# Kernel tuning notes

Measured on AMD Instinct MI355X. Metric: run time of the kernel, lower is better.

The kernel has to match this reference:

```python
import jax, jax.numpy as jnp
import numpy as np

EPS = 1e-5

def _bn(z, g, b):
    # train-mode BatchNorm2d: batch stats over (B,H,W), biased variance
    mean = z.mean(axis=(0, 2, 3), keepdims=True)
    var = z.var(axis=(0, 2, 3), keepdims=True)
    return g[None, :, None, None] * (z - mean) * jax.lax.rsqrt(var + EPS) + b[None, :, None, None]

def _conv1x1(x, w):
    # x: [B,C,H,W], w: [O,C] -> [B,O,H,W]
    return jnp.einsum('bchw,oc->bohw', x, w)

def _proj(x, w1, g1, b1, w2, g2, b2):
    z = _bn(_conv1x1(x, w1), g1, b1)
    return _bn(_conv1x1(z, w2), g2, b2)

def setup_inputs() -> dict:
    key = jax.random.key(0)
    ks = jax.random.split(key, 24)
    B, Cx, Cy, M, H, W = 4, 512, 256, 64, 64, 64
    f32 = jnp.float32
    def wmat(k, o, c):
        return jax.random.normal(k, (o, c), f32) * (c ** -0.5)
    def gamma(k, c):
        return 1.0 + 0.1 * jax.random.normal(k, (c,), f32)
    def beta(k, c):
        return 0.1 * jax.random.normal(k, (c,), f32)
    inp = {
        'x': jax.random.normal(ks[0], (B, Cx, H, W), f32),
        'y': jax.random.normal(ks[1], (B, Cy, H, W), f32),
        # f_self
        'ws1': wmat(ks[2], M, Cx), 'gs1': gamma(ks[3], M), 'bs1': beta(ks[4], M),
        'ws2': wmat(ks[5], M, M),  'gs2': gamma(ks[6], M), 'bs2': beta(ks[7], M),
        # f_x
        'wx1': wmat(ks[8], M, Cx), 'gx1': gamma(ks[9], M), 'bx1': beta(ks[10], M),
        'wx2': wmat(ks[11], M, M), 'gx2': gamma(ks[12], M), 'bx2': beta(ks[13], M),
        # f_y
        'wy1': wmat(ks[14], M, Cy), 'gy1': gamma(ks[15], M), 'by1': beta(ks[16], M),
        'wy2': wmat(ks[17], M, M),  'gy2': gamma(ks[18], M), 'by2': beta(ks[19], M),
        # f_up
        'wu': wmat(ks[20], Cx, M), 'gu': gamma(ks[21], Cx), 'bu': beta(ks[22], Cx),
    }
    return inp

def reference(x, y, ws1, gs1, bs1, ws2, gs2, bs2,
              wx1, gx1, bx1, wx2, gx2, bx2,
              wy1, gy1, by1, wy2, gy2, by2,
              wu, gu, bu):
    B, C, H, W = x.shape
    M = ws1.shape[0]
    N = H * W
    fself = _proj(x, ws1, gs1, bs1, ws2, gs2, bs2).reshape(B, M, N).transpose(0, 2, 1)  # [B,N,M]
    fx = _proj(x, wx1, gx1, bx1, wx2, gx2, bx2).reshape(B, M, N).transpose(0, 2, 1)      # [B,N,M]
    fy = _proj(y, wy1, gy1, by1, wy2, gy2, by2).reshape(B, M, N)                          # [B,M,N]
    sim = jnp.matmul(fx, fy)                  # [B,N,N]  (scale=False)
    attn = jax.nn.softmax(sim, axis=-1)
    fout = jnp.matmul(attn, fself)            # [B,N,M]
    fout = fout.transpose(0, 2, 1).reshape(B, M, H, W)
    out = _bn(_conv1x1(fout, wu), gu, bu)
    return x + out
```

## Files before the change

kernel.cpp:

```cpp
#include <hip/hip_runtime.h>
#include <hip/hip_fp16.h>
#include <cstdint>

constexpr int N_ = 4096;
constexpr float CNT = 16384.f;

typedef __attribute__((ext_vector_type(8))) _Float16 half8;
typedef __attribute__((ext_vector_type(4))) float f32x4;
union fragh { half8 h8; int i4[4]; };

__device__ inline int pkh(float a, float b) {
  union { __half2 h; int i; } u;
  u.h = __float22half2_rn(float2{a, b});
  return u.i;
}


__global__ __launch_bounds__(256) void conv1_k(
    const float* __restrict__ x, const float* __restrict__ y,
    const float* __restrict__ ws1, const float* __restrict__ wx1,
    const float* __restrict__ wy1,
    float* __restrict__ z1s, float* __restrict__ z1x, float* __restrict__ z1y,
    float* __restrict__ stats) {
  const int t = threadIdx.x;
  const int slice = blockIdx.x;
  const int b = slice >> 5;
  const int n0 = (slice & 31) * 128;
  const int branch = blockIdx.y;
  const float* A = branch == 2 ? y : x;
  const float* W = branch == 0 ? ws1 : (branch == 1 ? wx1 : wy1);
  float* out = branch == 0 ? z1s : (branch == 1 ? z1x : z1y);
  const int K = branch == 2 ? 256 : 512;
  float* st = stats + branch * 128;

  __shared__ float sA[32][132];
  __shared__ float sW[32][72];

  const int to = (t >> 5) * 8;
  const int tn = (t & 31) * 4;
  float acc[8][4];
#pragma unroll
  for (int i = 0; i < 8; ++i)
#pragma unroll
    for (int j = 0; j < 4; ++j) acc[i][j] = 0.f;

  const float* Ab = A + (size_t)b * K * N_ + n0;
#pragma unroll 1
  for (int k0 = 0; k0 < K; k0 += 32) {
    __syncthreads();
#pragma unroll
    for (int i = 0; i < 4; ++i) {
      int row = i * 8 + (t >> 5);
      float4 v = *(const float4*)&Ab[(size_t)(k0 + row) * N_ + tn];
      *(float4*)&sA[row][tn] = v;
    }
    {
      int o = t >> 2, kk = (t & 3) * 8;
      float4 w0 = *(const float4*)&W[(size_t)o * K + k0 + kk];
      float4 w1 = *(const float4*)&W[(size_t)o * K + k0 + kk + 4];
      sW[kk + 0][o] = w0.x; sW[kk + 1][o] = w0.y;
      sW[kk + 2][o] = w0.z; sW[kk + 3][o] = w0.w;
      sW[kk + 4][o] = w1.x; sW[kk + 5][o] = w1.y;
      sW[kk + 6][o] = w1.z; sW[kk + 7][o] = w1.w;
    }
    __syncthreads();
#pragma unroll
    for (int k = 0; k < 32; ++k) {
      float4 a = *(const float4*)&sA[k][tn];
      float4 w0 = *(const float4*)&sW[k][to];
      float4 w1 = *(const float4*)&sW[k][to + 4];
      float wv[8] = {w0.x, w0.y, w0.z, w0.w, w1.x, w1.y, w1.z, w1.w};
      float av[4] = {a.x, a.y, a.z, a.w};
#pragma unroll
      for (int i = 0; i < 8; ++i)
#pragma unroll
        for (int j = 0; j < 4; ++j) acc[i][j] += wv[i] * av[j];
    }
  }
  float* Cb = out + (size_t)b * 64 * N_ + n0;
#pragma unroll
  for (int i = 0; i < 8; ++i) {
    float4 v = {acc[i][0], acc[i][1], acc[i][2], acc[i][3]};
    *(float4*)&Cb[(size_t)(to + i) * N_ + tn] = v;
  }
#pragma unroll
  for (int i = 0; i < 8; ++i) {
    float s = acc[i][0] + acc[i][1] + acc[i][2] + acc[i][3];
    float q = acc[i][0] * acc[i][0] + acc[i][1] * acc[i][1] +
              acc[i][2] * acc[i][2] + acc[i][3] * acc[i][3];
#pragma unroll
    for (int d = 1; d < 32; d <<= 1) { s += __shfl_xor(s, d); q += __shfl_xor(q, d); }
    if ((t & 31) == 0) { atomicAdd(&st[to + i], s); atomicAdd(&st[64 + to + i], q); }
  }
}

__global__ __launch_bounds__(256) void conv2_k(
    const float* __restrict__ z1s, const float* __restrict__ z1x,
    const float* __restrict__ z1y,
    const float* __restrict__ ws2, const float* __restrict__ wx2,
    const float* __restrict__ wy2,
    const float* __restrict__ gs1, const float* __restrict__ bs1,
    const float* __restrict__ gx1, const float* __restrict__ bx1,
    const float* __restrict__ gy1, const float* __restrict__ by1,
    float* __restrict__ z2s, float* __restrict__ z2x, float* __restrict__ z2y,
    float* __restrict__ stats) {
  const int t = threadIdx.x;
  const int slice = blockIdx.x;
  const int b = slice >> 5;
  const int n0 = (slice & 31) * 128;
  const int branch = blockIdx.y;
  const float* A = branch == 0 ? z1s : (branch == 1 ? z1x : z1y);
  const float* W = branch == 0 ? ws2 : (branch == 1 ? wx2 : wy2);
  const float* g1 = branch == 0 ? gs1 : (branch == 1 ? gx1 : gy1);
  const float* b1 = branch == 0 ? bs1 : (branch == 1 ? bx1 : by1);
  float* out = branch == 0 ? z2s : (branch == 1 ? z2x : z2y);
  const float* stin = stats + branch * 128;
  float* stout = stats + (3 + branch) * 128;

  __shared__ float sA[32][132];
  __shared__ float sW[32][72];
  __shared__ float sc[64], sh[64];

  if (t < 64) {
    float mean = stin[t] * (1.f / CNT);
    float var = stin[64 + t] * (1.f / CNT) - mean * mean;
    float r = rsqrtf(var + 1e-5f);
    float s = g1[t] * r;
    sc[t] = s;
    sh[t] = b1[t] - mean * s;
  }

  const int to = (t >> 5) * 8;
  const int tn = (t & 31) * 4;
  float acc[8][4];
#pragma unroll
  for (int i = 0; i < 8; ++i)
#pragma unroll
    for (int j = 0; j < 4; ++j) acc[i][j] = 0.f;

  const float* Ab = A + (size_t)b * 64 * N_ + n0;
#pragma unroll 1
  for (int k0 = 0; k0 < 64; k0 += 32) {
    __syncthreads();
#pragma unroll
    for (int i = 0; i < 4; ++i) {
      int row = i * 8 + (t >> 5);
      float4 v = *(const float4*)&Ab[(size_t)(k0 + row) * N_ + tn];
      float s = sc[k0 + row], h = sh[k0 + row];
      v.x = v.x * s + h; v.y = v.y * s + h; v.z = v.z * s + h; v.w = v.w * s + h;
      *(float4*)&sA[row][tn] = v;
    }
    {
      int o = t >> 2, kk = (t & 3) * 8;
      float4 w0 = *(const float4*)&W[(size_t)o * 64 + k0 + kk];
      float4 w1 = *(const float4*)&W[(size_t)o * 64 + k0 + kk + 4];
      sW[kk + 0][o] = w0.x; sW[kk + 1][o] = w0.y;
      sW[kk + 2][o] = w0.z; sW[kk + 3][o] = w0.w;
      sW[kk + 4][o] = w1.x; sW[kk + 5][o] = w1.y;
      sW[kk + 6][o] = w1.z; sW[kk + 7][o] = w1.w;
    }
    __syncthreads();
#pragma unroll
    for (int k = 0; k < 32; ++k) {
      float4 a = *(const float4*)&sA[k][tn];
      float4 w0 = *(const float4*)&sW[k][to];
      float4 w1 = *(const float4*)&sW[k][to + 4];
      float wv[8] = {w0.x, w0.y, w0.z, w0.w, w1.x, w1.y, w1.z, w1.w};
      float av[4] = {a.x, a.y, a.z, a.w};
#pragma unroll
      for (int i = 0; i < 8; ++i)
#pragma unroll
        for (int j = 0; j < 4; ++j) acc[i][j] += wv[i] * av[j];
    }
  }
  float* Cb = out + (size_t)b * 64 * N_ + n0;
#pragma unroll
  for (int i = 0; i < 8; ++i) {
    float4 v = {acc[i][0], acc[i][1], acc[i][2], acc[i][3]};
    *(float4*)&Cb[(size_t)(to + i) * N_ + tn] = v;
  }
#pragma unroll
  for (int i = 0; i < 8; ++i) {
    float s = acc[i][0] + acc[i][1] + acc[i][2] + acc[i][3];
    float q = acc[i][0] * acc[i][0] + acc[i][1] * acc[i][1] +
              acc[i][2] * acc[i][2] + acc[i][3] * acc[i][3];
#pragma unroll
    for (int d = 1; d < 32; d <<= 1) { s += __shfl_xor(s, d); q += __shfl_xor(q, d); }
    if ((t & 31) == 0) { atomicAdd(&stout[to + i], s); atomicAdd(&stout[64 + to + i], q); }
  }
}

__global__ __launch_bounds__(256) void pack_k(
    const float* __restrict__ z2s, const float* __restrict__ z2x,
    const float* __restrict__ z2y,
    const float* __restrict__ gs2, const float* __restrict__ bs2,
    const float* __restrict__ gx2, const float* __restrict__ bx2,
    const float* __restrict__ gy2, const float* __restrict__ by2,
    int* __restrict__ Qh, int* __restrict__ Kf, int* __restrict__ Vf,
    const float* __restrict__ stats) {
  const int job = blockIdx.z;
  const int idx = blockIdx.x * 256 + threadIdx.x;
  const float* z2 = job == 0 ? z2x : (job == 1 ? z2y : z2s);
  const float* g2 = job == 0 ? gx2 : (job == 1 ? gy2 : gs2);
  const float* b2 = job == 0 ? bx2 : (job == 1 ? by2 : bs2);
  const float* st = stats + (job == 0 ? 4 : (job == 1 ? 5 : 3)) * 128;
  int* outp = job == 0 ? Qh : (job == 1 ? Kf : Vf);

  auto snorm = [&](int c, float& s, float& h) {
    float mean = st[c] * (1.f / CNT);
    float var = st[64 + c] * (1.f / CNT) - mean * mean;
    float r = rsqrtf(var + 1e-5f);
    s = g2[c] * r;
    h = b2[c] - mean * s;
  };
  if (job == 0) {
    int n = idx & 4095, c = (idx >> 12) & 31, b = idx >> 17;
    float s0, h0, s1, h1;
    snorm(2 * c, s0, h0);
    snorm(2 * c + 1, s1, h1);
    float v0 = z2[((size_t)b * 64 + 2 * c) * N_ + n] * s0 + h0;
    float v1 = z2[((size_t)b * 64 + 2 * c + 1) * N_ + n] * s1 + h1;
    outp[idx] = pkh(v0, v1);
  } else if (job == 1) {
    int n = idx & 4095, c = (idx >> 12) & 31, b = idx >> 17;
    float s0, h0, s1, h1;
    snorm(2 * c, s0, h0);
    snorm(2 * c + 1, s1, h1);
    float v0 = z2[((size_t)b * 64 + 2 * c) * N_ + n] * s0 + h0;
    float v1 = z2[((size_t)b * 64 + 2 * c + 1) * N_ + n] * s1 + h1;
    int t16 = n >> 4, la = n & 15, g = c >> 4, quad = (c & 15) >> 2, jj = c & 3;
    outp[(((b * 256 + t16) * 2 + g) * 64 + quad * 16 + la) * 4 + jj] = pkh(v0, v1);
  } else {
    int k = idx & 2047, ch = (idx >> 11) & 63, b = idx >> 17;
    float s0, h0;
    snorm(ch, s0, h0);
    float2 v = *(const float2*)&z2[((size_t)b * 64 + ch) * N_ + 2 * k];
    int kb = k >> 4, p = k & 15, quad = p >> 2, w = p & 3, mt = ch >> 4, la = ch & 15;
    outp[(((b * 128 + kb) * 4 + mt) * 64 + quad * 16 + la) * 4 + w] =
        pkh(v.x * s0 + h0, v.y * s0 + h0);
  }
}

__global__ __launch_bounds__(256, 4) void attn_k(const int* __restrict__ Qh,
                                                 const int* __restrict__ Kf,
                                                 const int* __restrict__ Vf,
                                                 float* __restrict__ fout) {
  const int tid = threadIdx.x;
  const int lane = tid & 63;
  const int wid = tid >> 6;
  const int la = lane & 15;
  const int quad = lane >> 4;
  const int b = blockIdx.x & 3;
  const int qbase = (blockIdx.x >> 2) * 16;
  const int* Qb = Qh + (size_t)b * 32 * N_;
  const int* Kb4 = Kf + (size_t)b * 131072;
  const int* Vb4 = Vf + (size_t)b * 131072;

  __shared__ union USm {
    int P16[4][16 * 20];
    struct { float O[4][16][69]; float M[4][16]; float L[4][16]; } e;
  } smu;
  int* myP = smu.P16[wid];

  fragh aq[2];
#pragma unroll
  for (int c = 0; c < 2; ++c)
#pragma unroll
    for (int j = 0; j < 4; ++j)
      aq[c].i4[j] = Qb[(size_t)(c * 16 + quad * 4 + j) * N_ + qbase + la];

  f32x4 o[4];
  float mrun = -3.0e38f, lrun = 0.f;
#pragma unroll
  for (int mt = 0; mt < 4; ++mt) o[mt] = f32x4{0.f, 0.f, 0.f, 0.f};

  const int jbeg = wid * (N_ / 4);
  const int jend = jbeg + N_ / 4;

  int4 ka[2][2], kb2[2][2];
#pragma unroll
  for (int nt = 0; nt < 2; ++nt)
#pragma unroll
    for (int g = 0; g < 2; ++g)
      ka[nt][g] = *(const int4*)&Kb4[((((jbeg >> 4) + nt) * 2 + g) * 64 + lane) * 4];

  auto body = [&](int j0, int4 (&kc)[2][2], int4 (&kn)[2][2]) {
    f32x4 s[2];
#pragma unroll
    for (int nt = 0; nt < 2; ++nt) {
      fragh k0, k1;
      k0.i4[0] = kc[nt][0].x; k0.i4[1] = kc[nt][0].y;
      k0.i4[2] = kc[nt][0].z; k0.i4[3] = kc[nt][0].w;
      k1.i4[0] = kc[nt][1].x; k1.i4[1] = kc[nt][1].y;
      k1.i4[2] = kc[nt][1].z; k1.i4[3] = kc[nt][1].w;
      f32x4 z = f32x4{0.f, 0.f, 0.f, 0.f};
      z = __builtin_amdgcn_mfma_f32_16x16x32_f16(k0.h8, aq[0].h8, z, 0, 0, 0);
      s[nt] = __builtin_amdgcn_mfma_f32_16x16x32_f16(k1.h8, aq[1].h8, z, 0, 0, 0);
    }
    int4 vv[4];
#pragma unroll
    for (int mt = 0; mt < 4; ++mt)
      vv[mt] = *(const int4*)&Vb4[(((j0 >> 5) * 4 + mt) * 64 + lane) * 4];
    const int nj = (j0 + 32 < jend) ? (j0 + 32) : jbeg;
#pragma unroll
    for (int nt = 0; nt < 2; ++nt)
#pragma unroll
      for (int g = 0; g < 2; ++g)
        kn[nt][g] = *(const int4*)&Kb4[((((nj >> 4) + nt) * 2 + g) * 64 + lane) * 4];
    float t0 = fmaxf(fmaxf(s[0][0], s[0][1]), fmaxf(s[0][2], s[0][3]));
    float t1 = fmaxf(fmaxf(s[1][0], s[1][1]), fmaxf(s[1][2], s[1][3]));
    float t = fmaxf(t0, t1);
    t = fmaxf(t, __shfl_xor(t, 16));
    t = fmaxf(t, __shfl_xor(t, 32));
    float mnew = fmaxf(mrun, t);
    float alpha = __expf(mrun - mnew);
    float p[2][4];
    float ps = 0.f;
#pragma unroll
    for (int nt = 0; nt < 2; ++nt)
#pragma unroll
      for (int r = 0; r < 4; ++r) {
        p[nt][r] = __expf(s[nt][r] - mnew);
        ps += p[nt][r];
      }
    ps += __shfl_xor(ps, 16);
    ps += __shfl_xor(ps, 32);
    lrun = lrun * alpha + ps;
    mrun = mnew;
#pragma unroll
    for (int nt = 0; nt < 2; ++nt) {
      myP[(nt * 8 + quad * 2 + 0) * 20 + la] = pkh(p[nt][0], p[nt][1]);
      myP[(nt * 8 + quad * 2 + 1) * 20 + la] = pkh(p[nt][2], p[nt][3]);
    }
    __asm__ __volatile__("s_waitcnt lgkmcnt(0)" ::: "memory");
    fragh pb;
#pragma unroll
    for (int j = 0; j < 4; ++j) pb.i4[j] = myP[(quad * 4 + j) * 20 + la];
#pragma unroll
    for (int mt = 0; mt < 4; ++mt) {
      o[mt][0] *= alpha; o[mt][1] *= alpha;
      o[mt][2] *= alpha; o[mt][3] *= alpha;
    }
#pragma unroll
    for (int mt = 0; mt < 4; ++mt) {
      fragh vb;
      vb.i4[0] = vv[mt].x; vb.i4[1] = vv[mt].y;
      vb.i4[2] = vv[mt].z; vb.i4[3] = vv[mt].w;
      o[mt] = __builtin_amdgcn_mfma_f32_16x16x32_f16(vb.h8, pb.h8, o[mt], 0, 0, 0);
    }
  };

#pragma unroll 1
  for (int j0 = jbeg; j0 < jend; j0 += 64) {
    body(j0, ka, kb2);
    body(j0 + 32, kb2, ka);
  }

  __syncthreads();
  if (quad == 0) {
    smu.e.M[wid][la] = mrun;
    smu.e.L[wid][la] = lrun;
  }
#pragma unroll
  for (int mt = 0; mt < 4; ++mt)
#pragma unroll
    for (int r = 0; r < 4; ++r) smu.e.O[wid][la][mt * 16 + quad * 4 + r] = o[mt][r];
  __syncthreads();

#pragma unroll
  for (int t = 0; t < 4; ++t) {
    int oidx = t * 256 + tid;
    int m = oidx >> 4;
    int q = oidx & 15;
    float m0 = fmaxf(fmaxf(smu.e.M[0][q], smu.e.M[1][q]),
                     fmaxf(smu.e.M[2][q], smu.e.M[3][q]));
    float num = 0.f, den = 0.f;
#pragma unroll
    for (int w = 0; w < 4; ++w) {
      float wgt = __expf(smu.e.M[w][q] - m0);
      num += wgt * smu.e.O[w][q][m];
      den += wgt * smu.e.L[w][q];
    }
    fout[((size_t)b * 64 + m) * N_ + qbase + q] = num / den;
  }
}

__global__ __launch_bounds__(256) void convup_k(const float* __restrict__ fout,
                                                const float* __restrict__ wu,
                                                float* __restrict__ u,
                                                float* __restrict__ stats) {
  const int t = threadIdx.x;
  const int slice = blockIdx.x;
  const int b = slice >> 5;
  const int n0 = (slice & 31) * 128;
  const int o0 = blockIdx.y * 64;

  __shared__ float sA[32][132];
  __shared__ float sW[32][72];

  const int to = (t >> 5) * 8;
  const int tn = (t & 31) * 4;
  float acc[8][4];
#pragma unroll
  for (int i = 0; i < 8; ++i)
#pragma unroll
    for (int j = 0; j < 4; ++j) acc[i][j] = 0.f;

  const float* Ab = fout + (size_t)b * 64 * N_ + n0;
#pragma unroll 1
  for (int k0 = 0; k0 < 64; k0 += 32) {
    __syncthreads();
#pragma unroll
    for (int i = 0; i < 4; ++i) {
      int row = i * 8 + (t >> 5);
      float4 v = *(const float4*)&Ab[(size_t)(k0 + row) * N_ + tn];
      *(float4*)&sA[row][tn] = v;
    }
    {
      int o = t >> 2, kk = (t & 3) * 8;
      float4 w0 = *(const float4*)&wu[(size_t)(o0 + o) * 64 + k0 + kk];
      float4 w1 = *(const float4*)&wu[(size_t)(o0 + o) * 64 + k0 + kk + 4];
      sW[kk + 0][o] = w0.x; sW[kk + 1][o] = w0.y;
      sW[kk + 2][o] = w0.z; sW[kk + 3][o] = w0.w;
      sW[kk + 4][o] = w1.x; sW[kk + 5][o] = w1.y;
      sW[kk + 6][o] = w1.z; sW[kk + 7][o] = w1.w;
    }
    __syncthreads();
#pragma unroll
    for (int k = 0; k < 32; ++k) {
      float4 a = *(const float4*)&sA[k][tn];
      float4 w0 = *(const float4*)&sW[k][to];
      float4 w1 = *(const float4*)&sW[k][to + 4];
      float wv[8] = {w0.x, w0.y, w0.z, w0.w, w1.x, w1.y, w1.z, w1.w};
      float av[4] = {a.x, a.y, a.z, a.w};
#pragma unroll
      for (int i = 0; i < 8; ++i)
#pragma unroll
        for (int j = 0; j < 4; ++j) acc[i][j] += wv[i] * av[j];
    }
  }
  float* Cb = u + ((size_t)b * 512 + o0) * N_ + n0;
#pragma unroll
  for (int i = 0; i < 8; ++i) {
    float4 v = {acc[i][0], acc[i][1], acc[i][2], acc[i][3]};
    *(float4*)&Cb[(size_t)(to + i) * N_ + tn] = v;
  }
#pragma unroll
  for (int i = 0; i < 8; ++i) {
    float s = acc[i][0] + acc[i][1] + acc[i][2] + acc[i][3];
    float q = acc[i][0] * acc[i][0] + acc[i][1] * acc[i][1] +
              acc[i][2] * acc[i][2] + acc[i][3] * acc[i][3];
#pragma unroll
    for (int d = 1; d < 32; d <<= 1) { s += __shfl_xor(s, d); q += __shfl_xor(q, d); }
    if ((t & 31) == 0) {
      atomicAdd(&stats[768 + o0 + to + i], s);
      atomicAdd(&stats[1280 + o0 + to + i], q);
    }
  }
}

__global__ __launch_bounds__(256) void final_k(const float* __restrict__ x,
                                               const float* __restrict__ u,
                                               const float* __restrict__ gu,
                                               const float* __restrict__ bu,
                                               const float* __restrict__ stats,
                                               float* __restrict__ out) {
  size_t idx = (size_t)blockIdx.x * 256 + threadIdx.x;
  int c = (int)((idx >> 12) & 511);
  float mean = stats[768 + c] * (1.f / CNT);
  float var = stats[1280 + c] * (1.f / CNT) - mean * mean;
  float r = rsqrtf(var + 1e-5f);
  float s = gu[c] * r;
  float sh = bu[c] - mean * s;
  out[idx] = x[idx] + u[idx] * s + sh;
}

extern "C" void kernel_launch(void* const* d_in, const int* in_sizes, int n_in,
                              void* d_out, int out_size, void* d_ws, size_t ws_size,
                              hipStream_t stream) {
  const float* x = (const float*)d_in[0];
  const float* y = (const float*)d_in[1];
  const float* ws1 = (const float*)d_in[2];
  const float* gs1 = (const float*)d_in[3];
  const float* bs1 = (const float*)d_in[4];
  const float* ws2 = (const float*)d_in[5];
  const float* gs2 = (const float*)d_in[6];
  const float* bs2 = (const float*)d_in[7];
  const float* wx1 = (const float*)d_in[8];
  const float* gx1 = (const float*)d_in[9];
  const float* bx1 = (const float*)d_in[10];
  const float* wx2 = (const float*)d_in[11];
  const float* gx2 = (const float*)d_in[12];
  const float* bx2 = (const float*)d_in[13];
  const float* wy1 = (const float*)d_in[14];
  const float* gy1 = (const float*)d_in[15];
  const float* by1 = (const float*)d_in[16];
  const float* wy2 = (const float*)d_in[17];
  const float* gy2 = (const float*)d_in[18];
  const float* by2 = (const float*)d_in[19];
  const float* wu = (const float*)d_in[20];
  const float* gu = (const float*)d_in[21];
  const float* bu = (const float*)d_in[22];
  float* out = (float*)d_out;

  float* w = (float*)d_ws;
  const size_t M1 = 1048576;
  float* z1s = w + 0 * M1;
  float* z1x = w + 1 * M1;
  float* z1y = w + 2 * M1;
  float* z2s = w + 3 * M1;
  float* z2x = w + 4 * M1;
  float* z2y = w + 5 * M1;
  float* fout = w + 6 * M1;
  float* u = w + 7 * M1;
  int* Qh = (int*)(w + 15 * M1);
  int* Kf = Qh + 524288;
  int* Vf = Kf + 524288;
  float* stats = (float*)(Vf + 524288);

  hipMemsetAsync(stats, 0, 1792 * sizeof(float), stream);

  conv1_k<<<dim3(128, 3), dim3(256), 0, stream>>>(x, y, ws1, wx1, wy1, z1s, z1x,
                                                  z1y, stats);
  conv2_k<<<dim3(128, 3), dim3(256), 0, stream>>>(
      z1s, z1x, z1y, ws2, wx2, wy2, gs1, bs1, gx1, bx1, gy1, by1, z2s, z2x, z2y,
      stats);
  pack_k<<<dim3(2048, 1, 3), dim3(256), 0, stream>>>(z2s, z2x, z2y, gs2, bs2, gx2,
                                                     bx2, gy2, by2, Qh, Kf, Vf,
                                                     stats);
  attn_k<<<dim3(1024), dim3(256), 0, stream>>>(Qh, Kf, Vf, fout);
  convup_k<<<dim3(128, 8), dim3(256), 0, stream>>>(fout, wu, u, stats);
  final_k<<<dim3(32768), dim3(256), 0, stream>>>(x, u, gu, bu, stats, out);
}
```

Before: 365.8 us.

## Restructure 1x1 conv kernels to wave-uniform scalar weights with pretransposed, BN-folded weights

The three pointwise conv kernels drop the LDS-tiled register-blocked GEMM. Each lane now owns one pixel and each wave 16 output channels, reading weights from pretransposed global buffers at wave-uniform addresses so they can be served as scalar loads. Small prep kernels transpose the weights and fold the first BatchNorm scale and shift into conv2's weights and bias, which removes the per-element normalize. This cuts shared memory use and barriers but adds three extra launches and gives less reuse of activations per thread. The prepped weights live in workspace buffers that are overwritten later (u, fout, z1s), so correctness depends on that ordering.

```diff
diff --git a/kernel.cpp b/kernel.cpp
--- a/kernel.cpp
+++ b/kernel.cpp
@@ -16,177 +16,165 @@
 }
 
 
-__global__ __launch_bounds__(256) void conv1_k(
-    const float* __restrict__ x, const float* __restrict__ y,
-    const float* __restrict__ ws1, const float* __restrict__ wx1,
-    const float* __restrict__ wy1,
-    float* __restrict__ z1s, float* __restrict__ z1x, float* __restrict__ z1y,
-    float* __restrict__ stats) {
-  const int t = threadIdx.x;
-  const int slice = blockIdx.x;
-  const int b = slice >> 5;
-  const int n0 = (slice & 31) * 128;
-  const int branch = blockIdx.y;
-  const float* A = branch == 2 ? y : x;
-  const float* W = branch == 0 ? ws1 : (branch == 1 ? wx1 : wy1);
-  float* out = branch == 0 ? z1s : (branch == 1 ? z1x : z1y);
-  const int K = branch == 2 ? 256 : 512;
-  float* st = stats + branch * 128;
-
-  __shared__ float sA[32][132];
-  __shared__ float sW[32][72];
-
-  const int to = (t >> 5) * 8;
-  const int tn = (t & 31) * 4;
-  float acc[8][4];
-#pragma unroll
-  for (int i = 0; i < 8; ++i)
-#pragma unroll
-    for (int j = 0; j < 4; ++j) acc[i][j] = 0.f;
-
-  const float* Ab = A + (size_t)b * K * N_ + n0;
-#pragma unroll 1
-  for (int k0 = 0; k0 < K; k0 += 32) {
-    __syncthreads();
-#pragma unroll
-    for (int i = 0; i < 4; ++i) {
-      int row = i * 8 + (t >> 5);
-      float4 v = *(const float4*)&Ab[(size_t)(k0 + row) * N_ + tn];
-      *(float4*)&sA[row][tn] = v;
-    }
-    {
-      int o = t >> 2, kk = (t & 3) * 8;
-      float4 w0 = *(const float4*)&W[(size_t)o * K + k0 + kk];
-      float4 w1 = *(const float4*)&W[(size_t)o * K + k0 + kk + 4];
-      sW[kk + 0][o] = w0.x; sW[kk + 1][o] = w0.y;
-      sW[kk + 2][o] = w0.z; sW[kk + 3][o] = w0.w;
-      sW[kk + 4][o] = w1.x; sW[kk + 5][o] = w1.y;
-      sW[kk + 6][o] = w1.z; sW[kk + 7][o] = w1.w;
-    }
-    __syncthreads();
-#pragma unroll
-    for (int k = 0; k < 32; ++k) {
-      float4 a = *(const float4*)&sA[k][tn];
-      float4 w0 = *(const float4*)&sW[k][to];
-      float4 w1 = *(const float4*)&sW[k][to + 4];
-      float wv[8] = {w0.x, w0.y, w0.z, w0.w, w1.x, w1.y, w1.z, w1.w};
-      float av[4] = {a.x, a.y, a.z, a.w};
-#pragma unroll
-      for (int i = 0; i < 8; ++i)
-#pragma unroll
-        for (int j = 0; j < 4; ++j) acc[i][j] += wv[i] * av[j];
-    }
-  }
-  float* Cb = out + (size_t)b * 64 * N_ + n0;
-#pragma unroll
-  for (int i = 0; i < 8; ++i) {
-    float4 v = {acc[i][0], acc[i][1], acc[i][2], acc[i][3]};
-    *(float4*)&Cb[(size_t)(to + i) * N_ + tn] = v;
-  }
-#pragma unroll
-  for (int i = 0; i < 8; ++i) {
-    float s = acc[i][0] + acc[i][1] + acc[i][2] + acc[i][3];
-    float q = acc[i][0] * acc[i][0] + acc[i][1] * acc[i][1] +
-              acc[i][2] * acc[i][2] + acc[i][3] * acc[i][3];
-#pragma unroll
-    for (int d = 1; d < 32; d <<= 1) { s += __shfl_xor(s, d); q += __shfl_xor(q, d); }
-    if ((t & 31) == 0) { atomicAdd(&st[to + i], s); atomicAdd(&st[64 + to + i], q); }
-  }
-}
-
-__global__ __launch_bounds__(256) void conv2_k(
-    const float* __restrict__ z1s, const float* __restrict__ z1x,
-    const float* __restrict__ z1y,
+__global__ __launch_bounds__(256) void prep1_k(const float* __restrict__ ws1,
+                                               const float* __restrict__ wx1,
+                                               const float* __restrict__ wy1,
+                                               float* __restrict__ wt1) {
+  int e = blockIdx.x * 256 + threadIdx.x;
+  if (e < 32768) {
+    int k = e >> 6, o = e & 63;
+    wt1[e] = ws1[o * 512 + k];
+  } else if (e < 65536) {
+    int e2 = e - 32768;
+    int k = e2 >> 6, o = e2 & 63;
+    wt1[e] = wx1[o * 512 + k];
+  } else {
+    int e3 = e - 65536;
+    int k = e3 >> 6, o = e3 & 63;
+    wt1[e] = wy1[o * 256 + k];
+  }
+}
+
+__global__ __launch_bounds__(256) void prep2_k(
     const float* __restrict__ ws2, const float* __restrict__ wx2,
     const float* __restrict__ wy2,
     const float* __restrict__ gs1, const float* __restrict__ bs1,
     const float* __restrict__ gx1, const float* __restrict__ bx1,
     const float* __restrict__ gy1, const float* __restrict__ by1,
+    const float* __restrict__ stats, float* __restrict__ wt2) {
+  const int branch = blockIdx.x;
+  const int t = threadIdx.x;
+  const float* W = branch == 0 ? ws2 : (branch == 1 ? wx2 : wy2);
+  const float* g1 = branch == 0 ? gs1 : (branch == 1 ? gx1 : gy1);
+  const float* b1 = branch == 0 ? bs1 : (branch == 1 ? bx1 : by1);
+  const float* stin = stats + branch * 128;
+  float* outW = wt2 + branch * 4096;
+  float* outB = wt2 + 12288 + branch * 64;
+
+#pragma unroll
+  for (int i = 0; i < 16; ++i) {
+    int e = i * 256 + t;
+    int k = e >> 6, o = e & 63;
+    float mean = stin[k] * (1.f / CNT);
+    float var = stin[64 + k] * (1.f / CNT) - mean * mean;
+    float sc = g1[k] * rsqrtf(var + 1e-5f);
+    outW[e] = W[o * 64 + k] * sc;
+  }
+  if (t < 64) {
+    float s = 0.f;
+    for (int k = 0; k < 64; ++k) {
+      float mean = stin[k] * (1.f / CNT);
+      float var = stin[64 + k] * (1.f / CNT) - mean * mean;
+      float sc = g1[k] * rsqrtf(var + 1e-5f);
+      float sh = b1[k] - mean * sc;
+      s += W[t * 64 + k] * sh;
+    }
+    outB[t] = s;
+  }
+}
+
+__global__ __launch_bounds__(256) void prepu_k(const float* __restrict__ wu,
+                                               float* __restrict__ wut) {
+  int e = blockIdx.x * 256 + threadIdx.x;
+  int k = e >> 9, o = e & 511;
+  wut[e] = wu[o * 64 + k];
+}
+
+__global__ __launch_bounds__(256) void conv1_k(
+    const float* __restrict__ x, const float* __restrict__ y,
+    const float* __restrict__ wt1,
+    float* __restrict__ z1s, float* __restrict__ z1x, float* __restrict__ z1y,
+    float* __restrict__ stats) {
+  const int t = threadIdx.x;
+  const int lane = t & 63;
+  const int wave = __builtin_amdgcn_readfirstlane(t >> 6);
+  const int slice = blockIdx.x;
+  const int b = slice >> 6;
+  const int n0 = (slice & 63) * 64;
+  const int branch = blockIdx.y;
+  const float* A = branch == 2 ? y : x;
+  const float* Wt = wt1 + (branch == 0 ? 0 : (branch == 1 ? 32768 : 65536));
+  float* out = branch == 0 ? z1s : (branch == 1 ? z1x : z1y);
+  const int K = branch == 2 ? 256 : 512;
+  float* st = stats + branch * 128;
+  const int o0 = wave * 16;
+
+  float acc[16];
+#pragma unroll
+  for (int i = 0; i < 16; ++i) acc[i] = 0.f;
+
+  const float* Ap = A + (size_t)b * K * N_ + n0 + lane;
+#pragma unroll 1
+  for (int k0 = 0; k0 < K; k0 += 8) {
+    float a[8];
+#pragma unroll
+    for (int j = 0; j < 8; ++j) a[j] = Ap[(size_t)(k0 + j) * N_];
+#pragma unroll
+    for (int j = 0; j < 8; ++j) {
+      const float* wk = Wt + (k0 + j) * 64 + o0;
+#pragma unroll
+      for (int i = 0; i < 16; ++i) acc[i] = fmaf(wk[i], a[j], acc[i]);
+    }
+  }
+  float* Cb = out + ((size_t)b * 64 + o0) * N_ + n0 + lane;
+#pragma unroll
+  for (int i = 0; i < 16; ++i) Cb[(size_t)i * N_] = acc[i];
+#pragma unroll
+  for (int i = 0; i < 16; ++i) {
+    float s = acc[i];
+    float q = acc[i] * acc[i];
+#pragma unroll
+    for (int d = 1; d < 64; d <<= 1) { s += __shfl_xor(s, d); q += __shfl_xor(q, d); }
+    if (lane == 0) { atomicAdd(&st[o0 + i], s); atomicAdd(&st[64 + o0 + i], q); }
+  }
+}
+
+__global__ __launch_bounds__(256) void conv2_k(
+    const float* __restrict__ z1s, const float* __restrict__ z1x,
+    const float* __restrict__ z1y, const float* __restrict__ wt2,
     float* __restrict__ z2s, float* __restrict__ z2x, float* __restrict__ z2y,
     float* __restrict__ stats) {
   const int t = threadIdx.x;
+  const int lane = t & 63;
+  const int wave = __builtin_amdgcn_readfirstlane(t >> 6);
   const int slice = blockIdx.x;
-  const int b = slice >> 5;
-  const int n0 = (slice & 31) * 128;
+  const int b = slice >> 6;
+  const int n0 = (slice & 63) * 64;
   const int branch = blockIdx.y;
   const float* A = branch == 0 ? z1s : (branch == 1 ? z1x : z1y);
-  const float* W = branch == 0 ? ws2 : (branch == 1 ? wx2 : wy2);
-  const float* g1 = branch == 0 ? gs1 : (branch == 1 ? gx1 : gy1);
-  const float* b1 = branch == 0 ? bs1 : (branch == 1 ? bx1 : by1);
+  const float* Wt = wt2 + branch * 4096;
+  const float* bias = wt2 + 12288 + branch * 64;
   float* out = branch == 0 ? z2s : (branch == 1 ? z2x : z2y);
-  const float* stin = stats + branch * 128;
-  float* stout = stats + (3 + branch) * 128;
-
-  __shared__ float sA[32][132];
-  __shared__ float sW[32][72];
-  __shared__ float sc[64], sh[64];
-
-  if (t < 64) {
-    float mean = stin[t] * (1.f / CNT);
-    float var = stin[64 + t] * (1.f / CNT) - mean * mean;
-    float r = rsqrtf(var + 1e-5f);
-    float s = g1[t] * r;
-    sc[t] = s;
-    sh[t] = b1[t] - mean * s;
-  }
-
-  const int to = (t >> 5) * 8;
-  const int tn = (t & 31) * 4;
-  float acc[8][4];
-#pragma unroll
-  for (int i = 0; i < 8; ++i)
-#pragma unroll
-    for (int j = 0; j < 4; ++j) acc[i][j] = 0.f;
-
-  const float* Ab = A + (size_t)b * 64 * N_ + n0;
+  float* st = stats + (3 + branch) * 128;
+  const int o0 = wave * 16;
+
+  float acc[16];
+#pragma unroll
+  for (int i = 0; i < 16; ++i) acc[i] = bias[o0 + i];
+
+  const float* Ap = A + (size_t)b * 64 * N_ + n0 + lane;
 #pragma unroll 1
-  for (int k0 = 0; k0 < 64; k0 += 32) {
-    __syncthreads();
-#pragma unroll
-    for (int i = 0; i < 4; ++i) {
-      int row = i * 8 + (t >> 5);
-      float4 v = *(const float4*)&Ab[(size_t)(k0 + row) * N_ + tn];
-      float s = sc[k0 + row], h = sh[k0 + row];
-      v.x = v.x * s + h; v.y = v.y * s + h; v.z = v.z * s + h; v.w = v.w * s + h;
-      *(float4*)&sA[row][tn] = v;
-    }
-    {
-      int o = t >> 2, kk = (t & 3) * 8;
-      float4 w0 = *(const float4*)&W[(size_t)o * 64 + k0 + kk];
-      float4 w1 = *(const float4*)&W[(size_t)o * 64 + k0 + kk + 4];
-      sW[kk + 0][o] = w0.x; sW[kk + 1][o] = w0.y;
-      sW[kk + 2][o] = w0.z; sW[kk + 3][o] = w0.w;
-      sW[kk + 4][o] = w1.x; sW[kk + 5][o] = w1.y;
-      sW[kk + 6][o] = w1.z; sW[kk + 7][o] = w1.w;
-    }
-    __syncthreads();
-#pragma unroll
-    for (int k = 0; k < 32; ++k) {
-      float4 a = *(const float4*)&sA[k][tn];
-      float4 w0 = *(const float4*)&sW[k][to];
-      float4 w1 = *(const float4*)&sW[k][to + 4];
-      float wv[8] = {w0.x, w0.y, w0.z, w0.w, w1.x, w1.y, w1.z, w1.w};
-      float av[4] = {a.x, a.y, a.z, a.w};
-#pragma unroll
-      for (int i = 0; i < 8; ++i)
-#pragma unroll
-        for (int j = 0; j < 4; ++j) acc[i][j] += wv[i] * av[j];
-    }
-  }
-  float* Cb = out + (size_t)b * 64 * N_ + n0;
-#pragma unroll
-  for (int i = 0; i < 8; ++i) {
-    float4 v = {acc[i][0], acc[i][1], acc[i][2], acc[i][3]};
-    *(float4*)&Cb[(size_t)(to + i) * N_ + tn] = v;
-  }
-#pragma unroll
-  for (int i = 0; i < 8; ++i) {
-    float s = acc[i][0] + acc[i][1] + acc[i][2] + acc[i][3];
-    float q = acc[i][0] * acc[i][0] + acc[i][1] * acc[i][1] +
-              acc[i][2] * acc[i][2] + acc[i][3] * acc[i][3];
-#pragma unroll
-    for (int d = 1; d < 32; d <<= 1) { s += __shfl_xor(s, d); q += __shfl_xor(q, d); }
-    if ((t & 31) == 0) { atomicAdd(&stout[to + i], s); atomicAdd(&stout[64 + to + i], q); }
+  for (int k0 = 0; k0 < 64; k0 += 8) {
+    float a[8];
+#pragma unroll
+    for (int j = 0; j < 8; ++j) a[j] = Ap[(size_t)(k0 + j) * N_];
+#pragma unroll
+    for (int j = 0; j < 8; ++j) {
+      const float* wk = Wt + (k0 + j) * 64 + o0;
+#pragma unroll
+      for (int i = 0; i < 16; ++i) acc[i] = fmaf(wk[i], a[j], acc[i]);
+    }
+  }
+  float* Cb = out + ((size_t)b * 64 + o0) * N_ + n0 + lane;
+#pragma unroll
+  for (int i = 0; i < 16; ++i) Cb[(size_t)i * N_] = acc[i];
+#pragma unroll
+  for (int i = 0; i < 16; ++i) {
+    float s = acc[i];
+    float q = acc[i] * acc[i];
+#pragma unroll
+    for (int d = 1; d < 64; d <<= 1) { s += __shfl_xor(s, d); q += __shfl_xor(q, d); }
+    if (lane == 0) { atomicAdd(&st[o0 + i], s); atomicAdd(&st[64 + o0 + i], q); }
   }
 }
 
@@ -386,75 +374,46 @@
 }
 
 __global__ __launch_bounds__(256) void convup_k(const float* __restrict__ fout,
-                                                const float* __restrict__ wu,
+                                                const float* __restrict__ wut,
                                                 float* __restrict__ u,
                                                 float* __restrict__ stats) {
   const int t = threadIdx.x;
+  const int lane = t & 63;
+  const int wave = __builtin_amdgcn_readfirstlane(t >> 6);
   const int slice = blockIdx.x;
-  const int b = slice >> 5;
-  const int n0 = (slice & 31) * 128;
-  const int o0 = blockIdx.y * 64;
-
-  __shared__ float sA[32][132];
-  __shared__ float sW[32][72];
-
-  const int to = (t >> 5) * 8;
-  const int tn = (t & 31) * 4;
-  float acc[8][4];
-#pragma unroll
-  for (int i = 0; i < 8; ++i)
-#pragma unroll
-    for (int j = 0; j < 4; ++j) acc[i][j] = 0.f;
-
-  const float* Ab = fout + (size_t)b * 64 * N_ + n0;
+  const int b = slice >> 6;
+  const int n0 = (slice & 63) * 64;
+  const int o0 = blockIdx.y * 64 + wave * 16;
+
+  float acc[16];
+#pragma unroll
+  for (int i = 0; i < 16; ++i) acc[i] = 0.f;
+
+  const float* Ap = fout + (size_t)b * 64 * N_ + n0 + lane;
 #pragma unroll 1
-  for (int k0 = 0; k0 < 64; k0 += 32) {
-    __syncthreads();
-#pragma unroll
-    for (int i = 0; i < 4; ++i) {
-      int row = i * 8 + (t >> 5);
-      float4 v = *(const float4*)&Ab[(size_t)(k0 + row) * N_ + tn];
-      *(float4*)&sA[row][tn] = v;
-    }
-    {
-      int o = t >> 2, kk = (t & 3) * 8;
-      float4 w0 = *(const float4*)&wu[(size_t)(o0 + o) * 64 + k0 + kk];
-      float4 w1 = *(const float4*)&wu[(size_t)(o0 + o) * 64 + k0 + kk + 4];
-      sW[kk + 0][o] = w0.x; sW[kk + 1][o] = w0.y;
-      sW[kk + 2][o] = w0.z; sW[kk + 3][o] = w0.w;
-      sW[kk + 4][o] = w1.x; sW[kk + 5][o] = w1.y;
-      sW[kk + 6][o] = w1.z; sW[kk + 7][o] = w1.w;
-    }
-    __syncthreads();
-#pragma unroll
-    for (int k = 0; k < 32; ++k) {
-      float4 a = *(const float4*)&sA[k][tn];
-      float4 w0 = *(const float4*)&sW[k][to];
-      float4 w1 = *(const float4*)&sW[k][to + 4];
-      float wv[8] = {w0.x, w0.y, w0.z, w0.w, w1.x, w1.y, w1.z, w1.w};
-      float av[4] = {a.x, a.y, a.z, a.w};
-#pragma unroll
-      for (int i = 0; i < 8; ++i)
-#pragma unroll
-        for (int j = 0; j < 4; ++j) acc[i][j] += wv[i] * av[j];
-    }
-  }
-  float* Cb = u + ((size_t)b * 512 + o0) * N_ + n0;
-#pragma unroll
-  for (int i = 0; i < 8; ++i) {
-    float4 v = {acc[i][0], acc[i][1], acc[i][2], acc[i][3]};
-    *(float4*)&Cb[(size_t)(to + i) * N_ + tn] = v;
-  }
-#pragma unroll
-  for (int i = 0; i < 8; ++i) {
-    float s = acc[i][0] + acc[i][1] + acc[i][2] + acc[i][3];
-    float q = acc[i][0] * acc[i][0] + acc[i][1] * acc[i][1] +
-              acc[i][2] * acc[i][2] + acc[i][3] * acc[i][3];
-#pragma unroll
-    for (int d = 1; d < 32; d <<= 1) { s += __shfl_xor(s, d); q += __shfl_xor(q, d); }
-    if ((t & 31) == 0) {
-      atomicAdd(&stats[768 + o0 + to + i], s);
-      atomicAdd(&stats[1280 + o0 + to + i], q);
+  for (int k0 = 0; k0 < 64; k0 += 8) {
+    float a[8];
+#pragma unroll
+    for (int j = 0; j < 8; ++j) a[j] = Ap[(size_t)(k0 + j) * N_];
+#pragma unroll
+    for (int j = 0; j < 8; ++j) {
+      const float* wk = wut + (k0 + j) * 512 + o0;
+#pragma unroll
+      for (int i = 0; i < 16; ++i) acc[i] = fmaf(wk[i], a[j], acc[i]);
+    }
+  }
+  float* Cb = u + ((size_t)b * 512 + o0) * N_ + n0 + lane;
+#pragma unroll
+  for (int i = 0; i < 16; ++i) Cb[(size_t)i * N_] = acc[i];
+#pragma unroll
+  for (int i = 0; i < 16; ++i) {
+    float s = acc[i];
+    float q = acc[i] * acc[i];
+#pragma unroll
+    for (int d = 1; d < 64; d <<= 1) { s += __shfl_xor(s, d); q += __shfl_xor(q, d); }
+    if (lane == 0) {
+      atomicAdd(&stats[768 + o0 + i], s);
+      atomicAdd(&stats[1280 + o0 + i], q);
     }
   }
 }
@@ -517,18 +476,23 @@
   int* Kf = Qh + 524288;
   int* Vf = Kf + 524288;
   float* stats = (float*)(Vf + 524288);
+  float* wt1 = u;
+  float* wt2 = fout;
+  float* wut = z1s;
 
   hipMemsetAsync(stats, 0, 1792 * sizeof(float), stream);
 
-  conv1_k<<<dim3(128, 3), dim3(256), 0, stream>>>(x, y, ws1, wx1, wy1, z1s, z1x,
-                                                  z1y, stats);
-  conv2_k<<<dim3(128, 3), dim3(256), 0, stream>>>(
-      z1s, z1x, z1y, ws2, wx2, wy2, gs1, bs1, gx1, bx1, gy1, by1, z2s, z2x, z2y,
-      stats);
+  prep1_k<<<dim3(320), dim3(256), 0, stream>>>(ws1, wx1, wy1, wt1);
+  conv1_k<<<dim3(256, 3), dim3(256), 0, stream>>>(x, y, wt1, z1s, z1x, z1y, stats);
+  prep2_k<<<dim3(3), dim3(256), 0, stream>>>(ws2, wx2, wy2, gs1, bs1, gx1, bx1,
+                                             gy1, by1, stats, wt2);
+  conv2_k<<<dim3(256, 3), dim3(256), 0, stream>>>(z1s, z1x, z1y, wt2, z2s, z2x,
+                                                  z2y, stats);
+  prepu_k<<<dim3(128), dim3(256), 0, stream>>>(wu, wut);
   pack_k<<<dim3(2048, 1, 3), dim3(256), 0, stream>>>(z2s, z2x, z2y, gs2, bs2, gx2,
                                                      bx2, gy2, by2, Qh, Kf, Vf,
                                                      stats);
   attn_k<<<dim3(1024), dim3(256), 0, stream>>>(Qh, Kf, Vf, fout);
-  convup_k<<<dim3(128, 8), dim3(256), 0, stream>>>(fout, wu, u, stats);
+  convup_k<<<dim3(256, 8), dim3(256), 0, stream>>>(fout, wut, u, stats);
   final_k<<<dim3(32768), dim3(256), 0, stream>>>(x, u, gu, bu, stats, out);
 }
```

Measured after the change: 788.3 us. 116% more time.
